# Kernel tuning notes

Hardware: AMD Instinct MI355X
Metric: run time of the kernel (lower is better)

## Reference

```python
import jax, jax.numpy as jnp
import numpy as np

NUM_HEADS = 12

def setup_inputs() -> dict:
    key = jax.random.key(0)
    k1, k2, k3, k4 = jax.random.split(key, 4)
    B, N, C = 64, 197, 768
    x = jax.random.normal(k1, (B, N, C), dtype=jnp.float32)
    w_qkv = jax.random.normal(k2, (3 * C, C), dtype=jnp.float32) * (C ** -0.5)
    w_proj = jax.random.normal(k3, (C, C), dtype=jnp.float32) * (C ** -0.5)
    b_proj = jax.random.normal(k4, (C,), dtype=jnp.float32) * 0.01
    return {"x": x, "w_qkv": w_qkv, "w_proj": w_proj, "b_proj": b_proj}

def reference(x, w_qkv, w_proj, b_proj):
    B, N, C = x.shape
    H = NUM_HEADS
    hd = C // H
    scale = hd ** -0.5
    # qkv linear (no bias): [B,N,3C] -> [3,B,H,N,hd]
    qkv = jnp.einsum('bnc,dc->bnd', x, w_qkv).reshape(B, N, 3, H, hd)
    qkv = jnp.transpose(qkv, (2, 0, 3, 1, 4))
    q, k, v = qkv[0], qkv[1], qkv[2]
    # full attention matrix [B,H,N,N] (materialized, matching the original)
    attn = jax.nn.softmax(jnp.einsum('bhnd,bhmd->bhnm', q, k) * scale, axis=-1)
    # CLS-token attention stats: mean over heads of attn row 0 (patch tokens) -> [B, N-1]
    global_attn = jnp.mean(attn[:, :, 0, 1:], axis=1)
    out = jnp.einsum('bhnm,bhmd->bhnd', attn, v)          # [B,H,N,hd]
    out = jnp.transpose(out, (0, 2, 1, 3)).reshape(B, N, C)
    out = jnp.einsum('bnc,dc->bnd', out, w_proj) + b_proj
    return out, global_attn
```

## Files before the change

### kernel.cpp

```cpp
#include <hip/hip_runtime.h>
#include <math.h>

#define B_   64
#define N_   197
#define C_   768
#define H_   12
#define HD_  64
#define BH_  (B_ * H_)
#define M_   (B_ * N_)

typedef _Float16 half8 __attribute__((ext_vector_type(8)));
typedef float    f32x4 __attribute__((ext_vector_type(4)));

#define MLDS 40

#define XH_OFF   0u
#define WQH_OFF  19365888u
#define WPH_OFF  22904832u
#define QH_OFF   24084480u
#define KH_OFF   43450368u
#define VH_OFF   62816256u
#define OH_OFF   82182144u
#define P0_OFF   101548032u
#define WS_BYTES 102150144u

__device__ __forceinline__ half8 h8zero() {
    half8 z;
    #pragma unroll
    for (int i = 0; i < 8; ++i) z[i] = (_Float16)0;
    return z;
}

__global__ void k_ws_too_small(float* out, float ws_bytes) { out[0] = -ws_bytes; }

__global__ __launch_bounds__(256) void k_cvt(const float* __restrict__ src,
                                             _Float16* __restrict__ dst, int n8) {
    const int i = blockIdx.x * blockDim.x + threadIdx.x;
    if (i >= n8) return;
    float4 f0 = *(const float4*)(src + (size_t)i * 8);
    float4 f1 = *(const float4*)(src + (size_t)i * 8 + 4);
    half8 h;
    h[0]=(_Float16)f0.x; h[1]=(_Float16)f0.y; h[2]=(_Float16)f0.z; h[3]=(_Float16)f0.w;
    h[4]=(_Float16)f1.x; h[5]=(_Float16)f1.y; h[6]=(_Float16)f1.z; h[7]=(_Float16)f1.w;
    *(half8*)(dst + (size_t)i * 8) = h;
}

__device__ __forceinline__ void mfma_nt_core_h(const _Float16* __restrict__ A,
                                               const _Float16* __restrict__ B,
                                               int M, int K, int m0, int n0,
                                               _Float16* As, _Float16* Bs,
                                               f32x4 (&acc)[4][4]) {
    const int tid  = threadIdx.x;
    const int r    = tid >> 1;
    const int c0   = (tid & 1) << 4;
    const int wave = tid >> 6, lane = tid & 63;
    const int wr   = (wave >> 1) << 6;
    const int wc   = (wave & 1) << 6;
    const int ln   = lane & 15, kq = lane >> 4;

    const int  ag   = m0 + r;
    const bool aval = ag < M;
    const _Float16* Ap = A + (size_t)(aval ? ag : 0) * K + c0;
    const _Float16* Bp = B + (size_t)(n0 + r) * K + c0;

    half8 a0 = *(const half8*)(Ap),     a1 = *(const half8*)(Ap + 8);
    half8 b0 = *(const half8*)(Bp),     b1 = *(const half8*)(Bp + 8);
    if (!aval) { a0 = h8zero(); a1 = h8zero(); }

    for (int k0 = 0; k0 < K; k0 += 32) {
        __syncthreads();
        *(half8*)&As[r * MLDS + c0]     = a0;
        *(half8*)&As[r * MLDS + c0 + 8] = a1;
        *(half8*)&Bs[r * MLDS + c0]     = b0;
        *(half8*)&Bs[r * MLDS + c0 + 8] = b1;
        __syncthreads();
        if (k0 + 32 < K) {
            a0 = *(const half8*)(Ap + k0 + 32); a1 = *(const half8*)(Ap + k0 + 40);
            b0 = *(const half8*)(Bp + k0 + 32); b1 = *(const half8*)(Bp + k0 + 40);
            if (!aval) { a0 = h8zero(); a1 = h8zero(); }
        }
        half8 af[4], bf[4];
        #pragma unroll
        for (int t = 0; t < 4; ++t) {
            af[t] = *(const half8*)&As[(wr + t * 16 + ln) * MLDS + kq * 8];
            bf[t] = *(const half8*)&Bs[(wc + t * 16 + ln) * MLDS + kq * 8];
        }
        #pragma unroll
        for (int i = 0; i < 4; ++i)
            #pragma unroll
            for (int j = 0; j < 4; ++j)
                acc[i][j] = __builtin_amdgcn_mfma_f32_16x16x32_f16(af[i], bf[j], acc[i][j], 0, 0, 0);
    }
}

__global__ __launch_bounds__(256) void k_qkv_mfma(const _Float16* __restrict__ Xh,
                                                  const _Float16* __restrict__ Wq,
                                                  _Float16* __restrict__ Qh,
                                                  _Float16* __restrict__ Kh,
                                                  _Float16* __restrict__ Vh) {
    __shared__ _Float16 As[128 * MLDS];
    __shared__ _Float16 Bs[128 * MLDS];
    const int m0 = blockIdx.y << 7;
    const int n0 = blockIdx.x << 7;
    f32x4 acc[4][4] = {};
    mfma_nt_core_h(Xh, Wq, M_, C_, m0, n0, As, Bs, acc);

    const int lane = threadIdx.x & 63;
    const int wave = threadIdx.x >> 6;
    const int wr = (wave >> 1) << 6, wc = (wave & 1) << 6;
    const int ln = lane & 15, kq = lane >> 4;
    #pragma unroll
    for (int mt = 0; mt < 4; ++mt) {
        #pragma unroll
        for (int i = 0; i < 4; ++i) {
            const int m = m0 + wr + mt * 16 + kq * 4 + i;
            if (m >= M_) continue;
            const int b = m / N_;
            const int n = m - b * N_;
            #pragma unroll
            for (int nt = 0; nt < 4; ++nt) {
                const int d  = n0 + wc + nt * 16 + ln;
                const int t3 = d / C_;
                const int rr = d - t3 * C_;
                const int h  = rr >> 6;
                const int e  = rr & 63;
                const size_t off = ((size_t)((b * H_ + h) * N_ + n)) * HD_ + e;
                const float v = acc[mt][nt][i];
                if      (t3 == 0) Qh[off] = (_Float16)(v * 0.125f);
                else if (t3 == 1) Kh[off] = (_Float16)v;
                else              Vh[off] = (_Float16)v;
            }
        }
    }
}

__global__ __launch_bounds__(256) void k_proj_mfma(const _Float16* __restrict__ Oh,
                                                   const _Float16* __restrict__ Wp,
                                                   const float* __restrict__ bias,
                                                   float* __restrict__ out) {
    __shared__ _Float16 As[128 * MLDS];
    __shared__ _Float16 Bs[128 * MLDS];
    const int m0 = blockIdx.y << 7;
    const int n0 = blockIdx.x << 7;
    f32x4 acc[4][4] = {};
    mfma_nt_core_h(Oh, Wp, M_, C_, m0, n0, As, Bs, acc);

    const int lane = threadIdx.x & 63;
    const int wave = threadIdx.x >> 6;
    const int wr = (wave >> 1) << 6, wc = (wave & 1) << 6;
    const int ln = lane & 15, kq = lane >> 4;
    float bv[4];
    #pragma unroll
    for (int nt = 0; nt < 4; ++nt) bv[nt] = bias[n0 + wc + nt * 16 + ln];
    #pragma unroll
    for (int mt = 0; mt < 4; ++mt) {
        #pragma unroll
        for (int i = 0; i < 4; ++i) {
            const int m = m0 + wr + mt * 16 + kq * 4 + i;
            if (m >= M_) continue;
            #pragma unroll
            for (int nt = 0; nt < 4; ++nt)
                out[(size_t)m * C_ + n0 + wc + nt * 16 + ln] = acc[mt][nt][i] + bv[nt];
        }
    }
}

__global__ __launch_bounds__(256) void k_attn(const _Float16* __restrict__ Qh,
                                              const _Float16* __restrict__ Kh,
                                              const _Float16* __restrict__ Vh,
                                              _Float16* __restrict__ Oh,
                                              float* __restrict__ P0) {
    __shared__ _Float16 lds[29824];
    _Float16* Ks = lds;
    _Float16* Pl = lds;
    _Float16* Vt = lds + 14976;

    const int bh = blockIdx.y, rt = blockIdx.x;
    const int b = bh / H_, h = bh - b * H_;
    const int tid = threadIdx.x, wave = tid >> 6, lane = tid & 63;
    const int ln = lane & 15, kq = lane >> 4;
    const size_t kvb = (size_t)bh * N_ * HD_;

    for (int idx = tid; idx < 208 * 8; idx += 256) {
        const int key = idx >> 3, c = (idx & 7) << 3;
        half8 v = (key < N_) ? *(const half8*)(Kh + kvb + (size_t)key * HD_ + c) : h8zero();
        *(half8*)&Ks[key * 72 + c] = v;
    }
    for (int idx = tid; idx < 197 * 8; idx += 256) {
        const int key = idx >> 3, c = (idx & 7) << 3;
        half8 v = *(const half8*)(Vh + kvb + (size_t)key * HD_ + c);
        #pragma unroll
        for (int j = 0; j < 8; ++j) Vt[(c + j) * 232 + key] = v[j];
    }
    for (int idx = tid; idx < 64 * 27; idx += 256) {
        const int d = idx / 27, k = 197 + (idx - d * 27);
        Vt[d * 232 + k] = (_Float16)0;
    }
    const int qrow = rt * 64 + wave * 16 + ln;
    const _Float16* Qp = Qh + kvb + (size_t)((qrow < N_) ? qrow : 0) * HD_ + kq * 8;
    half8 qf0 = *(const half8*)Qp;
    half8 qf1 = *(const half8*)(Qp + 32);
    __syncthreads();

    f32x4 acc[13] = {};
    #pragma unroll
    for (int c = 0; c < 13; ++c) {
        const _Float16* kp = &Ks[(c * 16 + ln) * 72 + kq * 8];
        half8 kf0 = *(const half8*)kp;
        half8 kf1 = *(const half8*)(kp + 32);
        acc[c] = __builtin_amdgcn_mfma_f32_16x16x32_f16(qf0, kf0, acc[c], 0, 0, 0);
        acc[c] = __builtin_amdgcn_mfma_f32_16x16x32_f16(qf1, kf1, acc[c], 0, 0, 0);
    }
    float inv4[4];
    #pragma unroll
    for (int r = 0; r < 4; ++r) {
        float m = -1e30f;
        #pragma unroll
        for (int c = 0; c < 13; ++c) {
            float x = ((c * 16 + ln) < N_) ? acc[c][r] : -1e30f;
            acc[c][r] = x;
            m = fmaxf(m, x);
        }
        m = fmaxf(m, __shfl_xor(m, 1)); m = fmaxf(m, __shfl_xor(m, 2));
        m = fmaxf(m, __shfl_xor(m, 4)); m = fmaxf(m, __shfl_xor(m, 8));
        float s = 0.f;
        #pragma unroll
        for (int c = 0; c < 13; ++c) { float e = __expf(acc[c][r] - m); acc[c][r] = e; s += e; }
        s += __shfl_xor(s, 1); s += __shfl_xor(s, 2);
        s += __shfl_xor(s, 4); s += __shfl_xor(s, 8);
        inv4[r] = 1.f / s;
    }
    __syncthreads();

    _Float16* Pw = Pl + wave * 16 * 232;
    #pragma unroll
    for (int c = 0; c < 13; ++c) {
        const int col = c * 16 + ln;
        #pragma unroll
        for (int r = 0; r < 4; ++r)
            Pw[(kq * 4 + r) * 232 + col] = (_Float16)(acc[c][r] * inv4[r]);
    }
    #pragma unroll
    for (int r = 0; r < 4; ++r) Pw[(kq * 4 + r) * 232 + 208 + ln] = (_Float16)0;

    if (rt == 0 && wave == 0 && kq == 0) {
        #pragma unroll
        for (int c = 0; c < 13; ++c) {
            const int col = c * 16 + ln;
            if (col >= 1 && col < N_) P0[(size_t)bh * 196 + col - 1] = acc[c][0] * inv4[0];
        }
    }
    __syncthreads();

    f32x4 o4[4] = {};
    for (int t = 0; t < 7; ++t) {
        half8 pf = *(const half8*)&Pw[ln * 232 + kq * 8 + 32 * t];
        #pragma unroll
        for (int n = 0; n < 4; ++n) {
            half8 vf = *(const half8*)&Vt[(n * 16 + ln) * 232 + kq * 8 + 32 * t];
            o4[n] = __builtin_amdgcn_mfma_f32_16x16x32_f16(pf, vf, o4[n], 0, 0, 0);
        }
    }
    const int g0 = rt * 64 + wave * 16 + kq * 4;
    #pragma unroll
    for (int r = 0; r < 4; ++r) {
        const int g = g0 + r;
        if (g >= N_) continue;
        _Float16* op = Oh + ((size_t)b * N_ + g) * C_ + h * HD_;
        #pragma unroll
        for (int n = 0; n < 4; ++n) op[n * 16 + ln] = (_Float16)o4[n][r];
    }
}

__global__ void k_gattn(const float* __restrict__ P0, float* __restrict__ out2) {
    const int idx = blockIdx.x * blockDim.x + threadIdx.x;
    const int b = idx / (N_ - 1), m = idx - b * (N_ - 1);
    float s = 0.f;
    #pragma unroll
    for (int h = 0; h < H_; ++h) s += P0[((size_t)(b * H_ + h)) * 196 + m];
    out2[idx] = s * (1.f / H_);
}

extern "C" void kernel_launch(void* const* d_in, const int* in_sizes, int n_in,
                              void* d_out, int out_size, void* d_ws, size_t ws_size,
                              hipStream_t stream) {
    const float* x      = (const float*)d_in[0];
    const float* w_qkv  = (const float*)d_in[1];
    const float* w_proj = (const float*)d_in[2];
    const float* b_proj = (const float*)d_in[3];
    float* out = (float*)d_out;
    char* ws   = (char*)d_ws;

    if (ws_size < (size_t)WS_BYTES) {
        k_ws_too_small<<<1, 1, 0, stream>>>(out, (float)ws_size);
        return;
    }

    _Float16* Xh  = (_Float16*)(ws + XH_OFF);
    _Float16* Wqh = (_Float16*)(ws + WQH_OFF);
    _Float16* Wph = (_Float16*)(ws + WPH_OFF);
    _Float16* Qh  = (_Float16*)(ws + QH_OFF);
    _Float16* Kh  = (_Float16*)(ws + KH_OFF);
    _Float16* Vh  = (_Float16*)(ws + VH_OFF);
    _Float16* Oh  = (_Float16*)(ws + OH_OFF);
    float*    P0  = (float*)   (ws + P0_OFF);

    k_cvt<<<4728, 256, 0, stream>>>(x,      Xh,  1210368);
    k_cvt<<< 864, 256, 0, stream>>>(w_qkv,  Wqh, 221184);
    k_cvt<<< 288, 256, 0, stream>>>(w_proj, Wph, 73728);

    k_qkv_mfma <<<dim3(18, 99), 256, 0, stream>>>(Xh, Wqh, Qh, Kh, Vh);
    k_attn     <<<dim3(4, BH_), 256, 0, stream>>>(Qh, Kh, Vh, Oh, P0);
    k_gattn    <<<dim3(49),     256, 0, stream>>>(P0, out + (size_t)M_ * C_);
    k_proj_mfma<<<dim3(6, 99),  256, 0, stream>>>(Oh, Wph, b_proj, out);
}
```

Measured before the change: 274.1 us.

## Use direct global-to-LDS swizzled GEMM loads and pre-transposed V for attention

The shared GEMM core now loads A and B tiles straight into LDS with global_load_lds. It uses an XOR-swizzled 64-wide K slab instead of register staging with padded rows, and drops the M-bound check by letting tail rows read neighbouring workspace. The QKV epilogue writes V already transposed into a zero-padded [bh, 64, 224] buffer, which a new small kernel pre-pads. The attention kernel then reads K and V fragments directly from global memory instead of staging and transposing them through LDS. This cuts LDS traffic and syncs, at the cost of scattered transposed stores in the QKV epilogue and uncached global fragment loads in attention.

```diff
diff --git a/kernel.cpp b/kernel.cpp
--- a/kernel.cpp
+++ b/kernel.cpp
@@ -12,23 +12,26 @@
 typedef _Float16 half8 __attribute__((ext_vector_type(8)));
 typedef float    f32x4 __attribute__((ext_vector_type(4)));
 
-#define MLDS 40
-
 #define XH_OFF   0u
 #define WQH_OFF  19365888u
 #define WPH_OFF  22904832u
 #define QH_OFF   24084480u
 #define KH_OFF   43450368u
-#define VH_OFF   62816256u
-#define OH_OFF   82182144u
-#define P0_OFF   101548032u
-#define WS_BYTES 102150144u
+#define VT_OFF   62816256u
+#define OH_OFF   84836352u
+#define P0_OFF   104202240u
+#define WS_BYTES 104804352u
 
 __device__ __forceinline__ half8 h8zero() {
     half8 z;
     #pragma unroll
     for (int i = 0; i < 8; ++i) z[i] = (_Float16)0;
     return z;
+}
+
+__device__ __forceinline__ void gld_lds16(const _Float16* g, _Float16* l) {
+    __builtin_amdgcn_global_load_lds((const __attribute__((address_space(1))) void*)g,
+                                     (__attribute__((address_space(3))) void*)l, 16, 0, 0);
 }
 
 __global__ void k_ws_too_small(float* out, float ws_bytes) { out[0] = -ws_bytes; }
@@ -45,51 +48,55 @@
     *(half8*)(dst + (size_t)i * 8) = h;
 }
 
-__device__ __forceinline__ void mfma_nt_core_h(const _Float16* __restrict__ A,
-                                               const _Float16* __restrict__ B,
-                                               int M, int K, int m0, int n0,
-                                               _Float16* As, _Float16* Bs,
-                                               f32x4 (&acc)[4][4]) {
+__global__ __launch_bounds__(256) void k_vpad(_Float16* __restrict__ Vt) {
+    const int i = blockIdx.x * 256 + threadIdx.x;
+    const int row = i >> 2, c = i & 3;
+    *(half8*)&Vt[(size_t)row * 224 + 192 + c * 8] = h8zero();
+}
+
+__device__ __forceinline__ void mfma_nt_core(const _Float16* __restrict__ A,
+                                             const _Float16* __restrict__ B,
+                                             int K, int m0, int n0,
+                                             _Float16* As, _Float16* Bs,
+                                             f32x4 (&acc)[4][4]) {
     const int tid  = threadIdx.x;
-    const int r    = tid >> 1;
-    const int c0   = (tid & 1) << 4;
     const int wave = tid >> 6, lane = tid & 63;
     const int wr   = (wave >> 1) << 6;
     const int wc   = (wave & 1) << 6;
     const int ln   = lane & 15, kq = lane >> 4;
 
-    const int  ag   = m0 + r;
-    const bool aval = ag < M;
-    const _Float16* Ap = A + (size_t)(aval ? ag : 0) * K + c0;
-    const _Float16* Bp = B + (size_t)(n0 + r) * K + c0;
-
-    half8 a0 = *(const half8*)(Ap),     a1 = *(const half8*)(Ap + 8);
-    half8 b0 = *(const half8*)(Bp),     b1 = *(const half8*)(Bp + 8);
-    if (!aval) { a0 = h8zero(); a1 = h8zero(); }
-
-    for (int k0 = 0; k0 < K; k0 += 32) {
+    const int srow = tid >> 3;
+    const int gc16 = (tid & 7) ^ (srow & 7);
+    const _Float16* Ab = A + (size_t)(m0 + srow) * K + gc16 * 8;
+    const _Float16* Bb = B + (size_t)(n0 + srow) * K + gc16 * 8;
+    const size_t rstep = (size_t)32 * K;
+    const int lbase = wave << 10;
+
+    const int sl0 = (kq ^ (ln & 7)) << 3;
+
+    for (int k0 = 0; k0 < K; k0 += 64) {
         __syncthreads();
-        *(half8*)&As[r * MLDS + c0]     = a0;
-        *(half8*)&As[r * MLDS + c0 + 8] = a1;
-        *(half8*)&Bs[r * MLDS + c0]     = b0;
-        *(half8*)&Bs[r * MLDS + c0 + 8] = b1;
+        #pragma unroll
+        for (int q = 0; q < 4; ++q) {
+            gld_lds16(Ab + k0 + q * rstep, (_Float16*)((char*)As + (q << 12) + lbase));
+            gld_lds16(Bb + k0 + q * rstep, (_Float16*)((char*)Bs + (q << 12) + lbase));
+        }
         __syncthreads();
-        if (k0 + 32 < K) {
-            a0 = *(const half8*)(Ap + k0 + 32); a1 = *(const half8*)(Ap + k0 + 40);
-            b0 = *(const half8*)(Bp + k0 + 32); b1 = *(const half8*)(Bp + k0 + 40);
-            if (!aval) { a0 = h8zero(); a1 = h8zero(); }
-        }
-        half8 af[4], bf[4];
-        #pragma unroll
-        for (int t = 0; t < 4; ++t) {
-            af[t] = *(const half8*)&As[(wr + t * 16 + ln) * MLDS + kq * 8];
-            bf[t] = *(const half8*)&Bs[(wc + t * 16 + ln) * MLDS + kq * 8];
-        }
-        #pragma unroll
-        for (int i = 0; i < 4; ++i)
+        #pragma unroll
+        for (int ks = 0; ks < 2; ++ks) {
+            const int so = sl0 ^ (ks << 5);
+            half8 af[4], bf[4];
             #pragma unroll
-            for (int j = 0; j < 4; ++j)
-                acc[i][j] = __builtin_amdgcn_mfma_f32_16x16x32_f16(af[i], bf[j], acc[i][j], 0, 0, 0);
+            for (int t = 0; t < 4; ++t) {
+                af[t] = *(const half8*)&As[((wr + t * 16 + ln) << 6) + so];
+                bf[t] = *(const half8*)&Bs[((wc + t * 16 + ln) << 6) + so];
+            }
+            #pragma unroll
+            for (int i = 0; i < 4; ++i)
+                #pragma unroll
+                for (int j = 0; j < 4; ++j)
+                    acc[i][j] = __builtin_amdgcn_mfma_f32_16x16x32_f16(af[i], bf[j], acc[i][j], 0, 0, 0);
+        }
     }
 }
 
@@ -97,13 +104,13 @@
                                                   const _Float16* __restrict__ Wq,
                                                   _Float16* __restrict__ Qh,
                                                   _Float16* __restrict__ Kh,
-                                                  _Float16* __restrict__ Vh) {
-    __shared__ _Float16 As[128 * MLDS];
-    __shared__ _Float16 Bs[128 * MLDS];
+                                                  _Float16* __restrict__ Vt) {
+    __shared__ _Float16 As[128 * 64];
+    __shared__ _Float16 Bs[128 * 64];
     const int m0 = blockIdx.y << 7;
     const int n0 = blockIdx.x << 7;
     f32x4 acc[4][4] = {};
-    mfma_nt_core_h(Xh, Wq, M_, C_, m0, n0, As, Bs, acc);
+    mfma_nt_core(Xh, Wq, C_, m0, n0, As, Bs, acc);
 
     const int lane = threadIdx.x & 63;
     const int wave = threadIdx.x >> 6;
@@ -124,11 +131,11 @@
                 const int rr = d - t3 * C_;
                 const int h  = rr >> 6;
                 const int e  = rr & 63;
-                const size_t off = ((size_t)((b * H_ + h) * N_ + n)) * HD_ + e;
+                const int bh = b * H_ + h;
                 const float v = acc[mt][nt][i];
-                if      (t3 == 0) Qh[off] = (_Float16)(v * 0.125f);
-                else if (t3 == 1) Kh[off] = (_Float16)v;
-                else              Vh[off] = (_Float16)v;
+                if      (t3 == 0) Qh[((size_t)bh * N_ + n) * HD_ + e] = (_Float16)(v * 0.125f);
+                else if (t3 == 1) Kh[((size_t)bh * N_ + n) * HD_ + e] = (_Float16)v;
+                else              Vt[((size_t)bh * HD_ + e) * 224 + n] = (_Float16)v;
             }
         }
     }
@@ -138,12 +145,12 @@
                                                    const _Float16* __restrict__ Wp,
                                                    const float* __restrict__ bias,
                                                    float* __restrict__ out) {
-    __shared__ _Float16 As[128 * MLDS];
-    __shared__ _Float16 Bs[128 * MLDS];
+    __shared__ _Float16 As[128 * 64];
+    __shared__ _Float16 Bs[128 * 64];
     const int m0 = blockIdx.y << 7;
     const int n0 = blockIdx.x << 7;
     f32x4 acc[4][4] = {};
-    mfma_nt_core_h(Oh, Wp, M_, C_, m0, n0, As, Bs, acc);
+    mfma_nt_core(Oh, Wp, C_, m0, n0, As, Bs, acc);
 
     const int lane = threadIdx.x & 63;
     const int wave = threadIdx.x >> 6;
@@ -167,47 +174,28 @@
 
 __global__ __launch_bounds__(256) void k_attn(const _Float16* __restrict__ Qh,
                                               const _Float16* __restrict__ Kh,
-                                              const _Float16* __restrict__ Vh,
+                                              const _Float16* __restrict__ Vt,
                                               _Float16* __restrict__ Oh,
                                               float* __restrict__ P0) {
-    __shared__ _Float16 lds[29824];
-    _Float16* Ks = lds;
-    _Float16* Pl = lds;
-    _Float16* Vt = lds + 14976;
-
+    __shared__ _Float16 Pl[4 * 16 * 232];
     const int bh = blockIdx.y, rt = blockIdx.x;
     const int b = bh / H_, h = bh - b * H_;
     const int tid = threadIdx.x, wave = tid >> 6, lane = tid & 63;
     const int ln = lane & 15, kq = lane >> 4;
     const size_t kvb = (size_t)bh * N_ * HD_;
-
-    for (int idx = tid; idx < 208 * 8; idx += 256) {
-        const int key = idx >> 3, c = (idx & 7) << 3;
-        half8 v = (key < N_) ? *(const half8*)(Kh + kvb + (size_t)key * HD_ + c) : h8zero();
-        *(half8*)&Ks[key * 72 + c] = v;
-    }
-    for (int idx = tid; idx < 197 * 8; idx += 256) {
-        const int key = idx >> 3, c = (idx & 7) << 3;
-        half8 v = *(const half8*)(Vh + kvb + (size_t)key * HD_ + c);
-        #pragma unroll
-        for (int j = 0; j < 8; ++j) Vt[(c + j) * 232 + key] = v[j];
-    }
-    for (int idx = tid; idx < 64 * 27; idx += 256) {
-        const int d = idx / 27, k = 197 + (idx - d * 27);
-        Vt[d * 232 + k] = (_Float16)0;
-    }
+    const size_t vtb = (size_t)bh * HD_ * 224;
+
     const int qrow = rt * 64 + wave * 16 + ln;
     const _Float16* Qp = Qh + kvb + (size_t)((qrow < N_) ? qrow : 0) * HD_ + kq * 8;
-    half8 qf0 = *(const half8*)Qp;
-    half8 qf1 = *(const half8*)(Qp + 32);
-    __syncthreads();
+    const half8 qf0 = *(const half8*)Qp;
+    const half8 qf1 = *(const half8*)(Qp + 32);
 
     f32x4 acc[13] = {};
     #pragma unroll
     for (int c = 0; c < 13; ++c) {
-        const _Float16* kp = &Ks[(c * 16 + ln) * 72 + kq * 8];
-        half8 kf0 = *(const half8*)kp;
-        half8 kf1 = *(const half8*)(kp + 32);
+        const _Float16* kp = Kh + kvb + (size_t)(c * 16 + ln) * HD_ + kq * 8;
+        const half8 kf0 = *(const half8*)kp;
+        const half8 kf1 = *(const half8*)(kp + 32);
         acc[c] = __builtin_amdgcn_mfma_f32_16x16x32_f16(qf0, kf0, acc[c], 0, 0, 0);
         acc[c] = __builtin_amdgcn_mfma_f32_16x16x32_f16(qf1, kf1, acc[c], 0, 0, 0);
     }
@@ -230,7 +218,6 @@
         s += __shfl_xor(s, 4); s += __shfl_xor(s, 8);
         inv4[r] = 1.f / s;
     }
-    __syncthreads();
 
     _Float16* Pw = Pl + wave * 16 * 232;
     #pragma unroll
@@ -253,11 +240,12 @@
     __syncthreads();
 
     f32x4 o4[4] = {};
+    #pragma unroll
     for (int t = 0; t < 7; ++t) {
-        half8 pf = *(const half8*)&Pw[ln * 232 + kq * 8 + 32 * t];
+        const half8 pf = *(const half8*)&Pw[ln * 232 + kq * 8 + 32 * t];
         #pragma unroll
         for (int n = 0; n < 4; ++n) {
-            half8 vf = *(const half8*)&Vt[(n * 16 + ln) * 232 + kq * 8 + 32 * t];
+            const half8 vf = *(const half8*)(Vt + vtb + (size_t)(n * 16 + ln) * 224 + kq * 8 + 32 * t);
             o4[n] = __builtin_amdgcn_mfma_f32_16x16x32_f16(pf, vf, o4[n], 0, 0, 0);
         }
     }
@@ -301,16 +289,17 @@
     _Float16* Wph = (_Float16*)(ws + WPH_OFF);
     _Float16* Qh  = (_Float16*)(ws + QH_OFF);
     _Float16* Kh  = (_Float16*)(ws + KH_OFF);
-    _Float16* Vh  = (_Float16*)(ws + VH_OFF);
+    _Float16* Vt  = (_Float16*)(ws + VT_OFF);
     _Float16* Oh  = (_Float16*)(ws + OH_OFF);
     float*    P0  = (float*)   (ws + P0_OFF);
 
     k_cvt<<<4728, 256, 0, stream>>>(x,      Xh,  1210368);
     k_cvt<<< 864, 256, 0, stream>>>(w_qkv,  Wqh, 221184);
     k_cvt<<< 288, 256, 0, stream>>>(w_proj, Wph, 73728);
-
-    k_qkv_mfma <<<dim3(18, 99), 256, 0, stream>>>(Xh, Wqh, Qh, Kh, Vh);
-    k_attn     <<<dim3(4, BH_), 256, 0, stream>>>(Qh, Kh, Vh, Oh, P0);
+    k_vpad<<<768, 256, 0, stream>>>(Vt);
+
+    k_qkv_mfma <<<dim3(18, 99), 256, 0, stream>>>(Xh, Wqh, Qh, Kh, Vt);
+    k_attn     <<<dim3(4, BH_), 256, 0, stream>>>(Qh, Kh, Vt, Oh, P0);
     k_gattn    <<<dim3(49),     256, 0, stream>>>(P0, out + (size_t)M_ * C_);
     k_proj_mfma<<<dim3(6, 99),  256, 0, stream>>>(Oh, Wph, b_proj, out);
 }
```

After: 291.3 us. 6.3% more time.
